# Kernel tuning notes

Measured on AMD Instinct MI355X. Metric: run time of the kernel, lower is better.

## Reference

```python
import jax, jax.numpy as jnp
import numpy as np

B, S, A, H, Z = 256, 512, 64, 1024, 256

def setup_inputs() -> dict:
    key = jax.random.key(0)
    ks = jax.random.split(key, 24)
    w = lambda k, shape: (jax.random.normal(k, shape, jnp.float32) * 0.02)
    inp = {
        "x": jax.random.randint(ks[0], (B, S), 0, A),
        "h0": jax.random.normal(ks[1], (B, H), jnp.float32),            # init_hidden randn
        "eps": jax.random.normal(ks[2], (S + 1, B, Z), jnp.float32),     # reparam noise per step + final
        "phi_x_w": w(ks[3], (H, A)),  "phi_x_b": jnp.zeros((H,), jnp.float32),
        "enc_w1": w(ks[4], (H, 2 * H)), "enc_b1": jnp.zeros((H,), jnp.float32),
        "enc_w2": w(ks[5], (Z, H)),     "enc_b2": jnp.zeros((Z,), jnp.float32),
        "pri_w1": w(ks[6], (H, H)),     "pri_b1": jnp.zeros((H,), jnp.float32),
        "pri_w2": w(ks[7], (Z, H)),     "pri_b2": jnp.zeros((Z,), jnp.float32),
        "phi_z_w": w(ks[8], (H, Z)),    "phi_z_b": jnp.zeros((H,), jnp.float32),
        "dec_w": w(ks[9], (H, 2 * H)),  "dec_b": jnp.zeros((H,), jnp.float32),
        "act_w": w(ks[10], (A, H)),     "act_b": jnp.zeros((A,), jnp.float32),
        "gru_wih": w(ks[11], (3 * H, 2 * H)), "gru_whh": w(ks[12], (3 * H, H)),
        "gru_bih": jnp.zeros((3 * H,), jnp.float32), "gru_bhh": jnp.zeros((3 * H,), jnp.float32),
    }
    return inp

def reference(x, h0, eps, phi_x_w, phi_x_b, enc_w1, enc_b1, enc_w2, enc_b2,
              pri_w1, pri_b1, pri_w2, pri_b2, phi_z_w, phi_z_b, dec_w, dec_b,
              act_w, act_b, gru_wih, gru_whh, gru_bih, gru_bhh):
    relu, sp = jax.nn.relu, jax.nn.softplus

    def gru_cell(xin, h):  # PyTorch GRU gate math
        gi = xin @ gru_wih.T + gru_bih
        gh = h @ gru_whh.T + gru_bhh
        ir, iz, inn = jnp.split(gi, 3, axis=-1)
        hr, hz, hn = jnp.split(gh, 3, axis=-1)
        r = jax.nn.sigmoid(ir + hr)
        zg = jax.nn.sigmoid(iz + hz)
        n = jnp.tanh(inn + r * hn)
        return (1.0 - zg) * n + zg * h

    def prior(h):
        p = relu(h @ pri_w1.T + pri_b1) @ pri_w2.T + pri_b2
        return p, sp(p)

    x_oh = jax.nn.one_hot(x, A, dtype=jnp.float32).transpose(1, 0, 2)  # [S,B,A]

    def step(carry, inp):
        h, kld = carry
        x_t, eps_t = inp
        px = relu(x_t @ phi_x_w.T + phi_x_b)                            # [B,H]
        enc = relu(jnp.concatenate([px, h], -1) @ enc_w1.T + enc_b1) @ enc_w2.T + enc_b2
        enc_std = sp(enc)
        pri_m, pri_std = prior(h)
        kld_el = (2 * jnp.log(pri_std) - 2 * jnp.log(enc_std)
                  + (enc_std ** 2 + (enc - pri_m) ** 2) / pri_std ** 2 - 1.0)
        kld = kld + 0.5 * jnp.sum(kld_el)
        z_t = eps_t * enc_std + enc                                     # reparam sample
        pz = relu(z_t @ phi_z_w.T + phi_z_b)
        h_new = gru_cell(jnp.concatenate([px, pz], -1), h)
        return (h_new, kld), None

    (h, kld), _ = jax.lax.scan(step, (h0, jnp.float32(0.0)), (x_oh, eps[:S]))

    pri_m, pri_std = prior(h)
    z_t = eps[S] * pri_std + pri_m
    pz = relu(z_t @ phi_z_w.T + phi_z_b)
    dec = relu(jnp.concatenate([pz, h], -1) @ dec_w.T + dec_b)
    pred_act = dec @ act_w.T + act_b
    return pred_act, kld
```

## Files before the change

kernel.cpp:

```cpp
#include <hip/hip_runtime.h>


typedef float f32x4 __attribute__((ext_vector_type(4)));
typedef __bf16 bf16x8 __attribute__((ext_vector_type(8)));

#define BB 256
#define SS 512
#define HH 1024
#define ZZ 256
#define AA 64
#define NWG 256

__device__ __forceinline__ float softplus_(float x) {
    return (x > 15.f) ? x : log1pf(expf(x));
}
__device__ __forceinline__ float sigmoid_(float x) {
    return 1.f / (1.f + expf(-x));
}

__device__ __forceinline__ void gbar(unsigned* bar, unsigned p, int wg) {
    __syncthreads();
    if (threadIdx.x == 0) {
        unsigned s = p & 7u;
        unsigned exp = (p >> 3) + 1u;
        unsigned* leaf = bar + (s * 8 + (wg >> 5)) * 16;
        unsigned* root = bar + (64 + s) * 16;
        unsigned* flag = bar + (72 + s) * 16;
        unsigned old = __hip_atomic_fetch_add(leaf, 1u, __ATOMIC_ACQ_REL, __HIP_MEMORY_SCOPE_AGENT);
        if (old == 32u * exp - 1u) {
            unsigned old2 = __hip_atomic_fetch_add(root, 1u, __ATOMIC_ACQ_REL, __HIP_MEMORY_SCOPE_AGENT);
            if (old2 == 8u * exp - 1u) {
                __hip_atomic_store(flag, exp, __ATOMIC_RELEASE, __HIP_MEMORY_SCOPE_AGENT);
            }
        }
        while (__hip_atomic_load(flag, __ATOMIC_ACQUIRE, __HIP_MEMORY_SCOPE_AGENT) < exp) {
            __builtin_amdgcn_s_sleep(2);
        }
    }
    __syncthreads();
}

__device__ __forceinline__ void xbar(unsigned* flags, int g, int rank, int ngrp,
                                     unsigned tok) {
    __syncthreads();
    if (threadIdx.x == 0)
        __hip_atomic_store(flags + g * 256 + rank, tok, __ATOMIC_RELAXED,
                           __HIP_MEMORY_SCOPE_AGENT);
    unsigned l = threadIdx.x & 63;
    unsigned* base = flags + g * 256;
    for (;;) {
        bool ok = true;
        for (int i = (int)l; i < ngrp; i += 64)
            ok &= (__hip_atomic_load(base + i, __ATOMIC_RELAXED,
                                     __HIP_MEMORY_SCOPE_AGENT) >= tok);
        if (__all(ok)) break;
        __builtin_amdgcn_s_sleep(2);
    }
    asm volatile("buffer_inv sc0" ::: "memory");
}

template<int MT, int NT>
__device__ __forceinline__ void wgemm(const __bf16* __restrict__ A, int lda, int mstride,
                                      const __bf16* __restrict__ B, int ldb, int nstride,
                                      int K, f32x4 (&acc)[MT][NT]) {
    int lane = threadIdx.x & 63;
    int rr = lane & 15;
    int ko = (lane >> 4) * 8;
    const __bf16* ap = A + rr * lda + ko;
    const __bf16* bp = B + rr * ldb + ko;
    #pragma unroll 2
    for (int k = 0; k < K; k += 32) {
        bf16x8 af[MT], bfr[NT];
        #pragma unroll
        for (int mt = 0; mt < MT; mt++) af[mt] = *(const bf16x8*)(ap + mt * mstride + k);
        #pragma unroll
        for (int nt = 0; nt < NT; nt++) bfr[nt] = *(const bf16x8*)(bp + nt * nstride + k);
        #pragma unroll
        for (int mt = 0; mt < MT; mt++)
            #pragma unroll
            for (int nt = 0; nt < NT; nt++)
                acc[mt][nt] = __builtin_amdgcn_mfma_f32_16x16x32_bf16(af[mt], bfr[nt], acc[mt][nt], 0, 0, 0);
    }
}


__global__ void k_zeroctl(unsigned* bar, unsigned* flags, unsigned* cnt, float* kldacc) {
    for (int i = threadIdx.x; i < 1280; i += 256) bar[i] = 0u;
    for (int i = threadIdx.x; i < 2048; i += 256) flags[i] = 0u;
    if (threadIdx.x < 8) cnt[threadIdx.x] = 0u;
    if (threadIdx.x == 0) *kldacc = 0.f;
}

__global__ void k_pack(const float* __restrict__ src, int src_ld, int col_off,
                       __bf16* __restrict__ dst, int cols, int total) {
    int i = blockIdx.x * 256 + threadIdx.x;
    if (i >= total) return;
    int r = i / cols, c = i - r * cols;
    dst[i] = (__bf16)src[r * src_ld + col_off + c];
}

__global__ void k_copyf(const float* __restrict__ s, float* __restrict__ d, int n) {
    int i = blockIdx.x * 256 + threadIdx.x;
    if (i < n) d[i] = s[i];
}

__global__ void k_px(const float* __restrict__ phi_x_w, const float* __restrict__ phi_x_b,
                     float* __restrict__ px) {
    int i = blockIdx.x * 256 + threadIdx.x;
    int a = i >> 10, hh = i & 1023;
    px[i] = fmaxf(phi_x_w[hh * AA + a] + phi_x_b[hh], 0.f);
}

__global__ __launch_bounds__(256) void k_tables(const float* __restrict__ enc_w1,
                                                const float* __restrict__ wih,
                                                const float* __restrict__ px,
                                                float* __restrict__ encpx,
                                                float* __restrict__ gipx) {
    __shared__ float spx[64][65];
    int tid = threadIdx.x;
    int cg = blockIdx.x * 4 + (tid >> 6);
    int a = tid & 63;
    const float* wrow = (cg < 1024) ? (enc_w1 + cg * 2048) : (wih + (cg - 1024) * 2048);
    float sum = 0.f;
    for (int k0 = 0; k0 < 1024; k0 += 64) {
        __syncthreads();
        for (int e = tid; e < 4096; e += 256)
            spx[e >> 6][e & 63] = px[((e >> 6) << 10) + k0 + (e & 63)];
        __syncthreads();
        #pragma unroll 8
        for (int kk = 0; kk < 64; kk++) sum += wrow[k0 + kk] * spx[a][kk];
    }
    if (cg < 1024) encpx[a * 1024 + cg] = sum;
    else gipx[a * 3072 + (cg - 1024)] = sum;
}


struct PArgs {
    const int* x; const float* eps;
    const __bf16 *WA, *W2, *WPZ, *WIH, *WHH, *WDEC, *WACT;
    const float *encpx, *gipx;
    const float *eb1, *pb1, *eb2, *pb2, *pzb, *decb, *actb, *bih, *bhh;
    float *hf0, *hf1; __bf16 *hb0, *hb1;
    __bf16 *hidcat, *zbuf, *pzbuf, *tailhid, *decbuf;
    float *gh; float *kldacc; unsigned *bar, *flags, *cnt;
    float* out;
};

__global__ __launch_bounds__(256) void k_persist(PArgs a) {
    int wg = blockIdx.x;
    int tid = threadIdx.x;
    int v = tid >> 6;
    int lane = tid & 63;
    int rr = lane & 15;
    int ko = (lane >> 4) * 8;
    int col = lane & 15, rq = (lane >> 4) * 4;
    float kl = 0.f;
    float* hf[2] = {a.hf0, a.hf1};
    __bf16* hb[2] = {a.hb0, a.hb1};

    __shared__ float lds2[4][2][256];
    __shared__ int sh_g, sh_rank, sh_ngrp;
    __shared__ float sh_kl[4];

    if (tid == 0) {
        unsigned xcc = __builtin_amdgcn_s_getreg((31 << 11) | (0 << 6) | 20) & 7u;
        sh_g = (int)xcc;
        sh_rank = (int)atomicAdd(a.cnt + xcc, 1u);
    }
    __syncthreads();
    int g = sh_g, rank = sh_rank;
    gbar(a.bar, 0, wg);
    if (tid == 0)
        sh_ngrp = (int)__hip_atomic_load(a.cnt + g, __ATOMIC_RELAXED,
                                         __HIP_MEMORY_SCOPE_AGENT);
    __syncthreads();
    int ngrp = sh_ngrp;
    int base_m = g * 32;

    unsigned tok = 1;

    for (int t = 0; t < SS; t++) {
        int cur = t & 1, nxt = cur ^ 1;

        for (int r = rank; r < 32; r += ngrp) {
            int mt = v >> 1;
            int nt0 = r * 10 + (v & 1) * 5;
            const __bf16* ap = hb[cur] + (size_t)(base_m + mt * 16 + rr) * HH + ko;
            const __bf16* bp[5];
            #pragma unroll
            for (int j = 0; j < 5; j++) {
                int n = (nt0 + j) * 16 + rr;
                bp[j] = ((n < 2048) ? (a.WA + (size_t)n * HH)
                                    : (a.WHH + (size_t)(n - 2048) * HH)) + ko;
            }
            f32x4 acc[5] = {};
            #pragma unroll 2
            for (int k = 0; k < HH; k += 32) {
                bf16x8 af = *(const bf16x8*)(ap + k);
                #pragma unroll
                for (int j = 0; j < 5; j++)
                    acc[j] = __builtin_amdgcn_mfma_f32_16x16x32_bf16(
                        af, *(const bf16x8*)(bp[j] + k), acc[j], 0, 0, 0);
            }
            int xb[4];
            #pragma unroll
            for (int i = 0; i < 4; i++)
                xb[i] = a.x[(base_m + mt * 16 + rq + i) * SS + t];
            #pragma unroll
            for (int j = 0; j < 5; j++) {
                int c0 = (nt0 + j) * 16 + col;
                if (c0 < 1024) {
                    float bias = a.eb1[c0];
                    #pragma unroll
                    for (int i = 0; i < 4; i++) {
                        int m = base_m + mt * 16 + rq + i;
                        float val = acc[j][i] + bias + a.encpx[xb[i] * 1024 + c0];
                        a.hidcat[m * 2048 + c0] = (__bf16)fmaxf(val, 0.f);
                    }
                } else if (c0 < 2048) {
                    float bias = a.pb1[c0 - 1024];
                    #pragma unroll
                    for (int i = 0; i < 4; i++) {
                        int m = base_m + mt * 16 + rq + i;
                        a.hidcat[m * 2048 + c0] = (__bf16)fmaxf(acc[j][i] + bias, 0.f);
                    }
                } else {
                    int gc = c0 - 2048;
                    #pragma unroll
                    for (int i = 0; i < 4; i++) {
                        int m = base_m + mt * 16 + rq + i;
                        a.gh[m * 3072 + gc] = acc[j][i];
                    }
                }
            }
        }
        xbar(a.flags, g, rank, ngrp, tok++);

        for (int r = rank; r < 32; r += ngrp) {
            int mtl = r >> 4, zsl = r & 15;
            const __bf16* ae_p = a.hidcat + (size_t)(base_m + mtl * 16 + rr) * 2048 + v * 256 + ko;
            const __bf16* ap_p = ae_p + 1024;
            const __bf16* be_p = a.W2 + (size_t)(zsl * 16 + rr) * HH + v * 256 + ko;
            const __bf16* bp_p = a.W2 + (size_t)(256 + zsl * 16 + rr) * HH + v * 256 + ko;
            f32x4 ae = {0.f,0.f,0.f,0.f}, av = {0.f,0.f,0.f,0.f};
            #pragma unroll
            for (int k = 0; k < 256; k += 32) {
                ae = __builtin_amdgcn_mfma_f32_16x16x32_bf16(
                    *(const bf16x8*)(ae_p + k), *(const bf16x8*)(be_p + k), ae, 0, 0, 0);
                av = __builtin_amdgcn_mfma_f32_16x16x32_bf16(
                    *(const bf16x8*)(ap_p + k), *(const bf16x8*)(bp_p + k), av, 0, 0, 0);
            }
            #pragma unroll
            for (int i = 0; i < 4; i++) {
                int idx = (rq + i) * 16 + col;
                lds2[v][0][idx] = ae[i];
                lds2[v][1][idx] = av[i];
            }
            __syncthreads();
            {
                float e = lds2[0][0][tid] + lds2[1][0][tid] + lds2[2][0][tid] + lds2[3][0][tid];
                float pv = lds2[0][1][tid] + lds2[1][1][tid] + lds2[2][1][tid] + lds2[3][1][tid];
                int m = base_m + mtl * 16 + (tid >> 4);
                int z = zsl * 16 + (tid & 15);
                float enc = e + a.eb2[z];
                float pri = pv + a.pb2[z];
                float es = softplus_(enc), ps = softplus_(pri);
                float d = enc - pri;
                kl += 2.f * (logf(ps) - logf(es)) + (es * es + d * d) / (ps * ps) - 1.f;
                const float* epst = a.eps + (size_t)t * BB * ZZ;
                a.zbuf[m * ZZ + z] = (__bf16)(epst[m * ZZ + z] * es + enc);
            }
            __syncthreads();
        }
        xbar(a.flags, g, rank, ngrp, tok++);

        for (int r = rank; r < 32; r += ngrp) {
            int mt = v >> 1;
            int nt = r * 2 + (v & 1);
            const __bf16* ap = a.zbuf + (size_t)(base_m + mt * 16 + rr) * ZZ + ko;
            const __bf16* bp = a.WPZ + (size_t)(nt * 16 + rr) * ZZ + ko;
            f32x4 acc = {0.f,0.f,0.f,0.f};
            #pragma unroll
            for (int k = 0; k < ZZ; k += 32)
                acc = __builtin_amdgcn_mfma_f32_16x16x32_bf16(
                    *(const bf16x8*)(ap + k), *(const bf16x8*)(bp + k), acc, 0, 0, 0);
            int n = nt * 16 + col;
            float b = a.pzb[n];
            #pragma unroll
            for (int i = 0; i < 4; i++) {
                int m = base_m + mt * 16 + rq + i;
                a.pzbuf[m * HH + n] = (__bf16)fmaxf(acc[i] + b, 0.f);
            }
        }
        xbar(a.flags, g, rank, ngrp, tok++);

        for (int r = rank; r < 32; r += ngrp) {
            int mt = v >> 1;
            int jt = r * 2 + (v & 1);
            const __bf16* ap = a.pzbuf + (size_t)(base_m + mt * 16 + rr) * HH + ko;
            const __bf16* bp0 = a.WIH + (size_t)(jt * 16 + rr) * HH + ko;
            const __bf16* bp1g = bp0 + (size_t)1024 * HH;
            const __bf16* bp2g = bp0 + (size_t)2048 * HH;
            f32x4 acc[3] = {};
            #pragma unroll 2
            for (int k = 0; k < HH; k += 32) {
                bf16x8 af = *(const bf16x8*)(ap + k);
                acc[0] = __builtin_amdgcn_mfma_f32_16x16x32_bf16(af, *(const bf16x8*)(bp0 + k), acc[0], 0, 0, 0);
                acc[1] = __builtin_amdgcn_mfma_f32_16x16x32_bf16(af, *(const bf16x8*)(bp1g + k), acc[1], 0, 0, 0);
                acc[2] = __builtin_amdgcn_mfma_f32_16x16x32_bf16(af, *(const bf16x8*)(bp2g + k), acc[2], 0, 0, 0);
            }
            int j = jt * 16 + col;
            float br = a.bih[j], bz2 = a.bih[1024 + j], bn = a.bih[2048 + j];
            float cr = a.bhh[j], cz = a.bhh[1024 + j], cn = a.bhh[2048 + j];
            #pragma unroll
            for (int i = 0; i < 4; i++) {
                int m = base_m + mt * 16 + rq + i;
                int xb = a.x[m * SS + t];
                const float* gp = a.gipx + xb * 3072;
                float gir = acc[0][i] + gp[j] + br;
                float giz = acc[1][i] + gp[1024 + j] + bz2;
                float gin = acc[2][i] + gp[2048 + j] + bn;
                float ghr = a.gh[m * 3072 + j] + cr;
                float ghz = a.gh[m * 3072 + 1024 + j] + cz;
                float ghn = a.gh[m * 3072 + 2048 + j] + cn;
                float rg = sigmoid_(gir + ghr);
                float zg = sigmoid_(giz + ghz);
                float nn = tanhf(gin + rg * ghn);
                float hv = (1.f - zg) * nn + zg * hf[cur][m * HH + j];
                hf[nxt][m * HH + j] = hv;
                hb[nxt][m * HH + j] = (__bf16)hv;
            }
        }
        xbar(a.flags, g, rank, ngrp, tok++);
    }

    for (int r = rank; r < 32; r += ngrp) {
        int mt = v >> 1, nt = r * 2 + (v & 1);
        f32x4 acc[1][1] = {};
        wgemm<1, 1>(hb[0] + (size_t)(base_m + mt * 16) * HH, HH, 0,
                    a.WA + (size_t)(1024 + nt * 16) * HH, HH, 0, HH, acc);
        int n = nt * 16 + col;
        float b = a.pb1[n];
        #pragma unroll
        for (int i = 0; i < 4; i++) {
            int m = base_m + mt * 16 + rq + i;
            a.tailhid[m * HH + n] = (__bf16)fmaxf(acc[0][0][i] + b, 0.f);
        }
    }
    xbar(a.flags, g, rank, ngrp, tok++);
    if (v == 0) {
        for (int r = rank; r < 32; r += ngrp) {
            int mtl = r >> 4, zt = r & 15;
            f32x4 apv[1][1] = {};
            wgemm<1, 1>(a.tailhid + (size_t)(base_m + mtl * 16) * HH, HH, 0,
                        a.W2 + (size_t)(256 + zt * 16) * HH, HH, 0, HH, apv);
            int z = zt * 16 + col;
            float bp = a.pb2[z];
            const float* epst = a.eps + (size_t)SS * BB * ZZ;
            #pragma unroll
            for (int i = 0; i < 4; i++) {
                int m = base_m + mtl * 16 + rq + i;
                float pri = apv[0][0][i] + bp;
                float ps = softplus_(pri);
                a.zbuf[m * ZZ + z] = (__bf16)(epst[m * ZZ + z] * ps + pri);
            }
        }
    }
    xbar(a.flags, g, rank, ngrp, tok++);
    for (int r = rank; r < 32; r += ngrp) {
        int mt = v >> 1, nt = r * 2 + (v & 1);
        f32x4 acc[1][1] = {};
        wgemm<1, 1>(a.zbuf + (size_t)(base_m + mt * 16) * ZZ, ZZ, 0,
                    a.WPZ + (size_t)(nt * 16) * ZZ, ZZ, 0, ZZ, acc);
        int n = nt * 16 + col;
        float b = a.pzb[n];
        #pragma unroll
        for (int i = 0; i < 4; i++) {
            int m = base_m + mt * 16 + rq + i;
            a.pzbuf[m * HH + n] = (__bf16)fmaxf(acc[0][0][i] + b, 0.f);
        }
    }
    xbar(a.flags, g, rank, ngrp, tok++);
    for (int r = rank; r < 32; r += ngrp) {
        int mt = v >> 1, nt = r * 2 + (v & 1);
        f32x4 acc[1][1] = {};
        wgemm<1, 1>(a.pzbuf + (size_t)(base_m + mt * 16) * HH, HH, 0,
                    a.WDEC + (size_t)(nt * 16) * 2048, 2048, 0, HH, acc);
        wgemm<1, 1>(hb[0] + (size_t)(base_m + mt * 16) * HH, HH, 0,
                    a.WDEC + (size_t)(nt * 16) * 2048 + 1024, 2048, 0, HH, acc);
        int n = nt * 16 + col;
        float b = a.decb[n];
        #pragma unroll
        for (int i = 0; i < 4; i++) {
            int m = base_m + mt * 16 + rq + i;
            a.decbuf[m * HH + n] = (__bf16)fmaxf(acc[0][0][i] + b, 0.f);
        }
    }
    xbar(a.flags, g, rank, ngrp, tok++);
    if (v == 0) {
        for (int r = rank; r < 32; r += ngrp) {
            if (r >= 8) continue;
            int mt = r >> 2, nt = r & 3;
            f32x4 acc[1][1] = {};
            wgemm<1, 1>(a.decbuf + (size_t)(base_m + mt * 16) * HH, HH, 0,
                        a.WACT + (size_t)(nt * 16) * HH, HH, 0, HH, acc);
            int n = nt * 16 + col;
            float b = a.actb[n];
            #pragma unroll
            for (int i = 0; i < 4; i++) {
                int m = base_m + mt * 16 + rq + i;
                a.out[m * AA + n] = acc[0][0][i] + b;
            }
        }
    }

    {
        float s = kl;
        #pragma unroll
        for (int off = 1; off < 64; off <<= 1) s += __shfl_xor(s, off);
        if (lane == 0) sh_kl[v] = s;
        __syncthreads();
        if (tid == 0) {
            float ws = sh_kl[0] + sh_kl[1] + sh_kl[2] + sh_kl[3];
            atomicAdd(a.kldacc, ws);
        }
    }
    gbar(a.bar, 1, wg);
    if (wg == 0 && tid == 0) {
        float s = __hip_atomic_load(a.kldacc, __ATOMIC_ACQUIRE, __HIP_MEMORY_SCOPE_AGENT);
        a.out[BB * AA] = 0.5f * s;
    }
}

extern "C" void kernel_launch(void* const* d_in, const int* in_sizes, int n_in,
                              void* d_out, int out_size, void* d_ws, size_t ws_size,
                              hipStream_t stream) {
    const int*   x       = (const int*)d_in[0];
    const float* h0      = (const float*)d_in[1];
    const float* eps     = (const float*)d_in[2];
    const float* phi_x_w = (const float*)d_in[3];
    const float* phi_x_b = (const float*)d_in[4];
    const float* enc_w1  = (const float*)d_in[5];
    const float* enc_b1  = (const float*)d_in[6];
    const float* enc_w2  = (const float*)d_in[7];
    const float* enc_b2  = (const float*)d_in[8];
    const float* pri_w1  = (const float*)d_in[9];
    const float* pri_b1  = (const float*)d_in[10];
    const float* pri_w2  = (const float*)d_in[11];
    const float* pri_b2  = (const float*)d_in[12];
    const float* phi_z_w = (const float*)d_in[13];
    const float* phi_z_b = (const float*)d_in[14];
    const float* dec_w   = (const float*)d_in[15];
    const float* dec_b   = (const float*)d_in[16];
    const float* act_w   = (const float*)d_in[17];
    const float* act_b   = (const float*)d_in[18];
    const float* gru_wih = (const float*)d_in[19];
    const float* gru_whh = (const float*)d_in[20];
    const float* gru_bih = (const float*)d_in[21];
    const float* gru_bhh = (const float*)d_in[22];

    char* p = (char*)d_ws;
    auto alloc = [&](size_t bytes) { char* r = p; p += (bytes + 255) & ~(size_t)255; return r; };

    __bf16* WA    = (__bf16*)alloc(2048 * 1024 * 2);
    __bf16* W2    = (__bf16*)alloc(512 * 1024 * 2);
    __bf16* WPZ   = (__bf16*)alloc(1024 * 256 * 2);
    __bf16* WIH   = (__bf16*)alloc(3072 * 1024 * 2);
    __bf16* WHH   = (__bf16*)alloc(3072 * 1024 * 2);
    __bf16* WDEC  = (__bf16*)alloc(1024 * 2048 * 2);
    __bf16* WACT  = (__bf16*)alloc(64 * 1024 * 2);
    float*  px    = (float*)alloc(64 * 1024 * 4);
    float*  encpx = (float*)alloc(64 * 1024 * 4);
    float*  gipx  = (float*)alloc(64 * 3072 * 4);
    float*  hf0   = (float*)alloc(BB * HH * 4);
    float*  hf1   = (float*)alloc(BB * HH * 4);
    __bf16* hb0   = (__bf16*)alloc(BB * HH * 2);
    __bf16* hb1   = (__bf16*)alloc(BB * HH * 2);
    __bf16* hidcat = (__bf16*)alloc(BB * 2048 * 2);
    __bf16* zbuf   = (__bf16*)alloc(BB * ZZ * 2);
    __bf16* pzbuf  = (__bf16*)alloc(BB * HH * 2);
    __bf16* tailhid = (__bf16*)alloc(BB * HH * 2);
    __bf16* decbuf  = (__bf16*)alloc(BB * HH * 2);
    float*  gh     = (float*)alloc(BB * 3072 * 4);
    unsigned* bar  = (unsigned*)alloc(1280 * 4);
    unsigned* flags = (unsigned*)alloc(2048 * 4);
    unsigned* cnt  = (unsigned*)alloc(64 * 4);
    float*  kldacc = (float*)alloc(256);

    auto pack = [&](const float* src, int src_ld, int off, __bf16* dst, int rows, int cols) {
        int total = rows * cols;
        k_pack<<<(total + 255) / 256, 256, 0, stream>>>(src, src_ld, off, dst, cols, total);
    };

    k_zeroctl<<<1, 256, 0, stream>>>(bar, flags, cnt, kldacc);
    pack(enc_w1, 2048, 1024, WA, 1024, 1024);
    pack(pri_w1, 1024, 0, WA + 1024 * 1024, 1024, 1024);
    pack(enc_w2, 1024, 0, W2, 256, 1024);
    pack(pri_w2, 1024, 0, W2 + 256 * 1024, 256, 1024);
    pack(phi_z_w, 256, 0, WPZ, 1024, 256);
    pack(gru_wih, 2048, 1024, WIH, 3072, 1024);
    pack(gru_whh, 1024, 0, WHH, 3072, 1024);
    pack(dec_w, 2048, 0, WDEC, 1024, 2048);
    pack(act_w, 1024, 0, WACT, 64, 1024);
    pack(h0, 1024, 0, hb0, 256, 1024);
    k_copyf<<<(BB * HH + 255) / 256, 256, 0, stream>>>(h0, hf0, BB * HH);
    k_px<<<(64 * 1024) / 256, 256, 0, stream>>>(phi_x_w, phi_x_b, px);
    k_tables<<<1024, 256, 0, stream>>>(enc_w1, gru_wih, px, encpx, gipx);

    PArgs pa;
    pa.x = x; pa.eps = eps;
// ... 16 lines not shown
```

Baseline: 29.21 ms.

## Double persistent workgroups and split recurrent GEMM tiles across more blocks

Raises the persistent grid from 256 to 512 workgroups with two blocks per CU, and rescales the tree barrier's leaf fan-in to match. The first per-step GEMM is repartitioned into 64 tiles of 5 column blocks, with waves alternating between 3 and 2 tiles. The GRU input GEMM splits K across wave pairs and reduces the halves through shared memory. The goal is more parallelism and latency hiding in each serial step, at the cost of more barrier participants, extra syncthreads, and register pressure from the 2-block launch bound.

After: 48.47 ms. 1.66x slower.

```diff
diff --git a/kernel.cpp b/kernel.cpp
--- a/kernel.cpp
+++ b/kernel.cpp
@@ -9,7 +9,7 @@
 #define HH 1024
 #define ZZ 256
 #define AA 64
-#define NWG 256
+#define NWG 512
 
 __device__ __forceinline__ float softplus_(float x) {
     return (x > 15.f) ? x : log1pf(expf(x));
@@ -23,11 +23,11 @@
     if (threadIdx.x == 0) {
         unsigned s = p & 7u;
         unsigned exp = (p >> 3) + 1u;
-        unsigned* leaf = bar + (s * 8 + (wg >> 5)) * 16;
+        unsigned* leaf = bar + (s * 8 + (wg >> 6)) * 16;
         unsigned* root = bar + (64 + s) * 16;
         unsigned* flag = bar + (72 + s) * 16;
         unsigned old = __hip_atomic_fetch_add(leaf, 1u, __ATOMIC_ACQ_REL, __HIP_MEMORY_SCOPE_AGENT);
-        if (old == 32u * exp - 1u) {
+        if (old == 64u * exp - 1u) {
             unsigned old2 = __hip_atomic_fetch_add(root, 1u, __ATOMIC_ACQ_REL, __HIP_MEMORY_SCOPE_AGENT);
             if (old2 == 8u * exp - 1u) {
                 __hip_atomic_store(flag, exp, __ATOMIC_RELEASE, __HIP_MEMORY_SCOPE_AGENT);
@@ -146,7 +146,7 @@
     float* out;
 };
 
-__global__ __launch_bounds__(256) void k_persist(PArgs a) {
+__global__ __launch_bounds__(256, 2) void k_persist(PArgs a) {
     int wg = blockIdx.x;
     int tid = threadIdx.x;
     int v = tid >> 6;
@@ -159,6 +159,7 @@
     __bf16* hb[2] = {a.hb0, a.hb1};
 
     __shared__ float lds2[4][2][256];
+    __shared__ float ldsP4[2][3][256];
     __shared__ int sh_g, sh_rank, sh_ngrp;
     __shared__ float sh_kl[4];
 
@@ -182,32 +183,46 @@
     for (int t = 0; t < SS; t++) {
         int cur = t & 1, nxt = cur ^ 1;
 
-        for (int r = rank; r < 32; r += ngrp) {
+        for (int r = rank; r < 64; r += ngrp) {
             int mt = v >> 1;
-            int nt0 = r * 10 + (v & 1) * 5;
+            int hv = (v ^ r) & 1;
+            int NT = hv ? 2 : 3;
+            int nt0 = r * 5 + (hv ? 3 : 0);
             const __bf16* ap = hb[cur] + (size_t)(base_m + mt * 16 + rr) * HH + ko;
-            const __bf16* bp[5];
-            #pragma unroll
-            for (int j = 0; j < 5; j++) {
-                int n = (nt0 + j) * 16 + rr;
-                bp[j] = ((n < 2048) ? (a.WA + (size_t)n * HH)
-                                    : (a.WHH + (size_t)(n - 2048) * HH)) + ko;
-            }
-            f32x4 acc[5] = {};
-            #pragma unroll 2
-            for (int k = 0; k < HH; k += 32) {
-                bf16x8 af = *(const bf16x8*)(ap + k);
-                #pragma unroll
-                for (int j = 0; j < 5; j++)
-                    acc[j] = __builtin_amdgcn_mfma_f32_16x16x32_bf16(
-                        af, *(const bf16x8*)(bp[j] + k), acc[j], 0, 0, 0);
+            int n0 = (nt0 + 0) * 16 + rr;
+            int n1 = (nt0 + 1) * 16 + rr;
+            const __bf16* bp0 = ((n0 < 2048) ? (a.WA + (size_t)n0 * HH)
+                                             : (a.WHH + (size_t)(n0 - 2048) * HH)) + ko;
+            const __bf16* bp1 = ((n1 < 2048) ? (a.WA + (size_t)n1 * HH)
+                                             : (a.WHH + (size_t)(n1 - 2048) * HH)) + ko;
+            const __bf16* bp2 = bp0;
+            if (NT == 3) {
+                int n2 = (nt0 + 2) * 16 + rr;
+                bp2 = ((n2 < 2048) ? (a.WA + (size_t)n2 * HH)
+                                   : (a.WHH + (size_t)(n2 - 2048) * HH)) + ko;
+            }
+            f32x4 acc[3] = {};
+            if (NT == 3) {
+                #pragma unroll 4
+                for (int k = 0; k < HH; k += 32) {
+                    bf16x8 af = *(const bf16x8*)(ap + k);
+                    acc[0] = __builtin_amdgcn_mfma_f32_16x16x32_bf16(af, *(const bf16x8*)(bp0 + k), acc[0], 0, 0, 0);
+                    acc[1] = __builtin_amdgcn_mfma_f32_16x16x32_bf16(af, *(const bf16x8*)(bp1 + k), acc[1], 0, 0, 0);
+                    acc[2] = __builtin_amdgcn_mfma_f32_16x16x32_bf16(af, *(const bf16x8*)(bp2 + k), acc[2], 0, 0, 0);
+                }
+            } else {
+                #pragma unroll 4
+                for (int k = 0; k < HH; k += 32) {
+                    bf16x8 af = *(const bf16x8*)(ap + k);
+                    acc[0] = __builtin_amdgcn_mfma_f32_16x16x32_bf16(af, *(const bf16x8*)(bp0 + k), acc[0], 0, 0, 0);
+                    acc[1] = __builtin_amdgcn_mfma_f32_16x16x32_bf16(af, *(const bf16x8*)(bp1 + k), acc[1], 0, 0, 0);
+                }
             }
             int xb[4];
             #pragma unroll
             for (int i = 0; i < 4; i++)
                 xb[i] = a.x[(base_m + mt * 16 + rq + i) * SS + t];
-            #pragma unroll
-            for (int j = 0; j < 5; j++) {
+            for (int j = 0; j < NT; j++) {
                 int c0 = (nt0 + j) * 16 + col;
                 if (c0 < 1024) {
                     float bias = a.eb1[c0];
@@ -294,42 +309,59 @@
         }
         xbar(a.flags, g, rank, ngrp, tok++);
 
-        for (int r = rank; r < 32; r += ngrp) {
+        for (int r = rank; r < 64; r += ngrp) {
             int mt = v >> 1;
-            int jt = r * 2 + (v & 1);
-            const __bf16* ap = a.pzbuf + (size_t)(base_m + mt * 16 + rr) * HH + ko;
-            const __bf16* bp0 = a.WIH + (size_t)(jt * 16 + rr) * HH + ko;
+            int kh = v & 1;
+            int jt = r;
+            const __bf16* ap = a.pzbuf + (size_t)(base_m + mt * 16 + rr) * HH + kh * 512 + ko;
+            const __bf16* bp0 = a.WIH + (size_t)(jt * 16 + rr) * HH + kh * 512 + ko;
             const __bf16* bp1g = bp0 + (size_t)1024 * HH;
             const __bf16* bp2g = bp0 + (size_t)2048 * HH;
             f32x4 acc[3] = {};
-            #pragma unroll 2
-            for (int k = 0; k < HH; k += 32) {
+            #pragma unroll 4
+            for (int k = 0; k < 512; k += 32) {
                 bf16x8 af = *(const bf16x8*)(ap + k);
                 acc[0] = __builtin_amdgcn_mfma_f32_16x16x32_bf16(af, *(const bf16x8*)(bp0 + k), acc[0], 0, 0, 0);
                 acc[1] = __builtin_amdgcn_mfma_f32_16x16x32_bf16(af, *(const bf16x8*)(bp1g + k), acc[1], 0, 0, 0);
                 acc[2] = __builtin_amdgcn_mfma_f32_16x16x32_bf16(af, *(const bf16x8*)(bp2g + k), acc[2], 0, 0, 0);
             }
-            int j = jt * 16 + col;
-            float br = a.bih[j], bz2 = a.bih[1024 + j], bn = a.bih[2048 + j];
-            float cr = a.bhh[j], cz = a.bhh[1024 + j], cn = a.bhh[2048 + j];
-            #pragma unroll
-            for (int i = 0; i < 4; i++) {
-                int m = base_m + mt * 16 + rq + i;
-                int xb = a.x[m * SS + t];
-                const float* gp = a.gipx + xb * 3072;
-                float gir = acc[0][i] + gp[j] + br;
-                float giz = acc[1][i] + gp[1024 + j] + bz2;
-                float gin = acc[2][i] + gp[2048 + j] + bn;
-                float ghr = a.gh[m * 3072 + j] + cr;
-                float ghz = a.gh[m * 3072 + 1024 + j] + cz;
-                float ghn = a.gh[m * 3072 + 2048 + j] + cn;
-                float rg = sigmoid_(gir + ghr);
-                float zg = sigmoid_(giz + ghz);
-                float nn = tanhf(gin + rg * ghn);
-                float hv = (1.f - zg) * nn + zg * hf[cur][m * HH + j];
-                hf[nxt][m * HH + j] = hv;
-                hb[nxt][m * HH + j] = (__bf16)hv;
-            }
+            if (kh) {
+                #pragma unroll
+                for (int g3 = 0; g3 < 3; g3++)
+                    #pragma unroll
+                    for (int i = 0; i < 4; i++)
+                        ldsP4[mt][g3][(rq + i) * 16 + col] = acc[g3][i];
+            }
+            __syncthreads();
+            if (!kh) {
+                #pragma unroll
+                for (int g3 = 0; g3 < 3; g3++)
+                    #pragma unroll
+                    for (int i = 0; i < 4; i++)
+                        acc[g3][i] += ldsP4[mt][g3][(rq + i) * 16 + col];
+                int j = jt * 16 + col;
+                float br = a.bih[j], bz2 = a.bih[1024 + j], bn = a.bih[2048 + j];
+                float cr = a.bhh[j], cz = a.bhh[1024 + j], cn = a.bhh[2048 + j];
+                #pragma unroll
+                for (int i = 0; i < 4; i++) {
+                    int m = base_m + mt * 16 + rq + i;
+                    int xb = a.x[m * SS + t];
+                    const float* gp = a.gipx + xb * 3072;
+                    float gir = acc[0][i] + gp[j] + br;
+                    float giz = acc[1][i] + gp[1024 + j] + bz2;
+                    float gin = acc[2][i] + gp[2048 + j] + bn;
+                    float ghr = a.gh[m * 3072 + j] + cr;
+                    float ghz = a.gh[m * 3072 + 1024 + j] + cz;
+                    float ghn = a.gh[m * 3072 + 2048 + j] + cn;
+                    float rg = sigmoid_(gir + ghr);
+                    float zg = sigmoid_(giz + ghz);
+                    float nn = tanhf(gin + rg * ghn);
+                    float hv2 = (1.f - zg) * nn + zg * hf[cur][m * HH + j];
+                    hf[nxt][m * HH + j] = hv2;
+                    hb[nxt][m * HH + j] = (__bf16)hv2;
+                }
+            }
+            __syncthreads();
         }
         xbar(a.flags, g, rank, ngrp, tok++);
     }
```

## Split K across waves with LDS reduction to reuse B fragments over two M tiles

Applied to the files above, without the earlier changes.

In the two big per-step GEMM phases (hidden projection and GRU input gates), each wave now covers both 16-row M tiles and half of K instead of one M tile and the full K. Each B fragment loaded from global memory therefore feeds two MFMAs. Partial sums are exchanged through a new 20KB LDS buffer and the epilogue work is split across the two K halves. This halves weight traffic per MFMA but adds LDS traffic, extra __syncthreads, and more accumulator registers. It also sets launch bounds to one block per CU.

Result: faster. 27.86 ms (-4.6%).

```diff
diff --git a/kernel.cpp b/kernel.cpp
--- a/kernel.cpp
+++ b/kernel.cpp
@@ -146,7 +146,7 @@
     float* out;
 };
 
-__global__ __launch_bounds__(256) void k_persist(PArgs a) {
+__global__ __launch_bounds__(256, 1) void k_persist(PArgs a) {
     int wg = blockIdx.x;
     int tid = threadIdx.x;
     int v = tid >> 6;
@@ -158,6 +158,7 @@
     float* hf[2] = {a.hf0, a.hf1};
     __bf16* hb[2] = {a.hb0, a.hb1};
 
+    __shared__ float ldsC[5120];
     __shared__ float lds2[4][2][256];
     __shared__ int sh_g, sh_rank, sh_ngrp;
     __shared__ float sh_kl[4];
@@ -183,56 +184,84 @@
         int cur = t & 1, nxt = cur ^ 1;
 
         for (int r = rank; r < 32; r += ngrp) {
-            int mt = v >> 1;
-            int nt0 = r * 10 + (v & 1) * 5;
-            const __bf16* ap = hb[cur] + (size_t)(base_m + mt * 16 + rr) * HH + ko;
+            int nh = v & 1, kh = v >> 1;
+            int nt0 = r * 10 + nh * 5;
+            const __bf16* ap0 = hb[cur] + (size_t)(base_m + rr) * HH + kh * 512 + ko;
+            const __bf16* ap1 = ap0 + (size_t)16 * HH;
             const __bf16* bp[5];
             #pragma unroll
             for (int j = 0; j < 5; j++) {
                 int n = (nt0 + j) * 16 + rr;
                 bp[j] = ((n < 2048) ? (a.WA + (size_t)n * HH)
-                                    : (a.WHH + (size_t)(n - 2048) * HH)) + ko;
-            }
-            f32x4 acc[5] = {};
-            #pragma unroll 2
-            for (int k = 0; k < HH; k += 32) {
-                bf16x8 af = *(const bf16x8*)(ap + k);
+                                    : (a.WHH + (size_t)(n - 2048) * HH)) + kh * 512 + ko;
+            }
+            f32x4 acc[2][5] = {};
+            #pragma unroll 4
+            for (int k = 0; k < 512; k += 32) {
+                bf16x8 a0 = *(const bf16x8*)(ap0 + k);
+                bf16x8 a1 = *(const bf16x8*)(ap1 + k);
                 #pragma unroll
-                for (int j = 0; j < 5; j++)
-                    acc[j] = __builtin_amdgcn_mfma_f32_16x16x32_bf16(
-                        af, *(const bf16x8*)(bp[j] + k), acc[j], 0, 0, 0);
-            }
-            int xb[4];
-            #pragma unroll
-            for (int i = 0; i < 4; i++)
-                xb[i] = a.x[(base_m + mt * 16 + rq + i) * SS + t];
-            #pragma unroll
-            for (int j = 0; j < 5; j++) {
+                for (int j = 0; j < 5; j++) {
+                    bf16x8 bb = *(const bf16x8*)(bp[j] + k);
+                    acc[0][j] = __builtin_amdgcn_mfma_f32_16x16x32_bf16(a0, bb, acc[0][j], 0, 0, 0);
+                    acc[1][j] = __builtin_amdgcn_mfma_f32_16x16x32_bf16(a1, bb, acc[1][j], 0, 0, 0);
+                }
+            }
+            {
+                int wlo = kh ? 0 : 3, whi = kh ? 3 : 5;
+                for (int j = wlo; j < whi; j++)
+                    #pragma unroll
+                    for (int mt = 0; mt < 2; mt++)
+                        #pragma unroll
+                        for (int i = 0; i < 4; i++)
+                            ldsC[((nh * 5 + j) * 2 + mt) * 256 + (rq + i) * 16 + col] = acc[mt][j][i];
+            }
+            int xbv[2][4];
+            #pragma unroll
+            for (int mt = 0; mt < 2; mt++)
+                #pragma unroll
+                for (int i = 0; i < 4; i++)
+                    xbv[mt][i] = a.x[(base_m + mt * 16 + rq + i) * SS + t];
+            __syncthreads();
+            int jlo = kh ? 3 : 0, jhi = kh ? 5 : 3;
+            for (int j = jlo; j < jhi; j++) {
+                #pragma unroll
+                for (int mt = 0; mt < 2; mt++)
+                    #pragma unroll
+                    for (int i = 0; i < 4; i++)
+                        acc[mt][j][i] += ldsC[((nh * 5 + j) * 2 + mt) * 256 + (rq + i) * 16 + col];
                 int c0 = (nt0 + j) * 16 + col;
                 if (c0 < 1024) {
                     float bias = a.eb1[c0];
                     #pragma unroll
-                    for (int i = 0; i < 4; i++) {
-                        int m = base_m + mt * 16 + rq + i;
-                        float val = acc[j][i] + bias + a.encpx[xb[i] * 1024 + c0];
-                        a.hidcat[m * 2048 + c0] = (__bf16)fmaxf(val, 0.f);
-                    }
+                    for (int mt = 0; mt < 2; mt++)
+                        #pragma unroll
+                        for (int i = 0; i < 4; i++) {
+                            int m = base_m + mt * 16 + rq + i;
+                            float val = acc[mt][j][i] + bias + a.encpx[xbv[mt][i] * 1024 + c0];
+                            a.hidcat[m * 2048 + c0] = (__bf16)fmaxf(val, 0.f);
+                        }
                 } else if (c0 < 2048) {
                     float bias = a.pb1[c0 - 1024];
                     #pragma unroll
-                    for (int i = 0; i < 4; i++) {
-                        int m = base_m + mt * 16 + rq + i;
-                        a.hidcat[m * 2048 + c0] = (__bf16)fmaxf(acc[j][i] + bias, 0.f);
-                    }
+                    for (int mt = 0; mt < 2; mt++)
+                        #pragma unroll
+                        for (int i = 0; i < 4; i++) {
+                            int m = base_m + mt * 16 + rq + i;
+                            a.hidcat[m * 2048 + c0] = (__bf16)fmaxf(acc[mt][j][i] + bias, 0.f);
+                        }
                 } else {
                     int gc = c0 - 2048;
                     #pragma unroll
-                    for (int i = 0; i < 4; i++) {
-                        int m = base_m + mt * 16 + rq + i;
-                        a.gh[m * 3072 + gc] = acc[j][i];
-                    }
+                    for (int mt = 0; mt < 2; mt++)
+                        #pragma unroll
+                        for (int i = 0; i < 4; i++) {
+                            int m = base_m + mt * 16 + rq + i;
+                            a.gh[m * 3072 + gc] = acc[mt][j][i];
+                        }
                 }
             }
+            __syncthreads();
         }
         xbar(a.flags, g, rank, ngrp, tok++);
 
@@ -295,41 +324,67 @@
         xbar(a.flags, g, rank, ngrp, tok++);
 
         for (int r = rank; r < 32; r += ngrp) {
-            int mt = v >> 1;
-            int jt = r * 2 + (v & 1);
-            const __bf16* ap = a.pzbuf + (size_t)(base_m + mt * 16 + rr) * HH + ko;
-            const __bf16* bp0 = a.WIH + (size_t)(jt * 16 + rr) * HH + ko;
+            int jh = v & 1, kh = v >> 1;
+            int jt = r * 2 + jh;
+            const __bf16* ap0 = a.pzbuf + (size_t)(base_m + rr) * HH + kh * 512 + ko;
+            const __bf16* ap1 = ap0 + (size_t)16 * HH;
+            const __bf16* bp0 = a.WIH + (size_t)(jt * 16 + rr) * HH + kh * 512 + ko;
             const __bf16* bp1g = bp0 + (size_t)1024 * HH;
             const __bf16* bp2g = bp0 + (size_t)2048 * HH;
-            f32x4 acc[3] = {};
-            #pragma unroll 2
-            for (int k = 0; k < HH; k += 32) {
-                bf16x8 af = *(const bf16x8*)(ap + k);
-                acc[0] = __builtin_amdgcn_mfma_f32_16x16x32_bf16(af, *(const bf16x8*)(bp0 + k), acc[0], 0, 0, 0);
-                acc[1] = __builtin_amdgcn_mfma_f32_16x16x32_bf16(af, *(const bf16x8*)(bp1g + k), acc[1], 0, 0, 0);
-                acc[2] = __builtin_amdgcn_mfma_f32_16x16x32_bf16(af, *(const bf16x8*)(bp2g + k), acc[2], 0, 0, 0);
-            }
-            int j = jt * 16 + col;
-            float br = a.bih[j], bz2 = a.bih[1024 + j], bn = a.bih[2048 + j];
-            float cr = a.bhh[j], cz = a.bhh[1024 + j], cn = a.bhh[2048 + j];
-            #pragma unroll
-            for (int i = 0; i < 4; i++) {
-                int m = base_m + mt * 16 + rq + i;
-                int xb = a.x[m * SS + t];
-                const float* gp = a.gipx + xb * 3072;
-                float gir = acc[0][i] + gp[j] + br;
-                float giz = acc[1][i] + gp[1024 + j] + bz2;
-                float gin = acc[2][i] + gp[2048 + j] + bn;
-                float ghr = a.gh[m * 3072 + j] + cr;
-                float ghz = a.gh[m * 3072 + 1024 + j] + cz;
-                float ghn = a.gh[m * 3072 + 2048 + j] + cn;
-                float rg = sigmoid_(gir + ghr);
-                float zg = sigmoid_(giz + ghz);
-                float nn = tanhf(gin + rg * ghn);
-                float hv = (1.f - zg) * nn + zg * hf[cur][m * HH + j];
-                hf[nxt][m * HH + j] = hv;
-                hb[nxt][m * HH + j] = (__bf16)hv;
-            }
+            f32x4 acc[2][3] = {};
+            #pragma unroll 4
+            for (int k = 0; k < 512; k += 32) {
+                bf16x8 a0 = *(const bf16x8*)(ap0 + k);
+                bf16x8 a1 = *(const bf16x8*)(ap1 + k);
+                bf16x8 b0 = *(const bf16x8*)(bp0 + k);
+                bf16x8 b1 = *(const bf16x8*)(bp1g + k);
+                bf16x8 b2 = *(const bf16x8*)(bp2g + k);
+                acc[0][0] = __builtin_amdgcn_mfma_f32_16x16x32_bf16(a0, b0, acc[0][0], 0, 0, 0);
+                acc[0][1] = __builtin_amdgcn_mfma_f32_16x16x32_bf16(a0, b1, acc[0][1], 0, 0, 0);
+                acc[0][2] = __builtin_amdgcn_mfma_f32_16x16x32_bf16(a0, b2, acc[0][2], 0, 0, 0);
+                acc[1][0] = __builtin_amdgcn_mfma_f32_16x16x32_bf16(a1, b0, acc[1][0], 0, 0, 0);
+                acc[1][1] = __builtin_amdgcn_mfma_f32_16x16x32_bf16(a1, b1, acc[1][1], 0, 0, 0);
+                acc[1][2] = __builtin_amdgcn_mfma_f32_16x16x32_bf16(a1, b2, acc[1][2], 0, 0, 0);
+            }
+            {
+                int mtW = kh ^ 1;
+                #pragma unroll
+                for (int g3 = 0; g3 < 3; g3++)
+                    #pragma unroll
+                    for (int i = 0; i < 4; i++)
+                        ldsC[((jh * 2 + mtW) * 3 + g3) * 256 + (rq + i) * 16 + col] = acc[mtW][g3][i];
+            }
+            __syncthreads();
+            {
+                int mt = kh;
+                #pragma unroll
+                for (int g3 = 0; g3 < 3; g3++)
+                    #pragma unroll
+                    for (int i = 0; i < 4; i++)
+                        acc[mt][g3][i] += ldsC[((jh * 2 + mt) * 3 + g3) * 256 + (rq + i) * 16 + col];
+                int j = jt * 16 + col;
+                float br = a.bih[j], bz2 = a.bih[1024 + j], bn = a.bih[2048 + j];
+                float cr = a.bhh[j], cz = a.bhh[1024 + j], cn = a.bhh[2048 + j];
+                #pragma unroll
+                for (int i = 0; i < 4; i++) {
+                    int m = base_m + mt * 16 + rq + i;
+                    int xb = a.x[m * SS + t];
+                    const float* gp = a.gipx + xb * 3072;
+                    float gir = acc[mt][0][i] + gp[j] + br;
+                    float giz = acc[mt][1][i] + gp[1024 + j] + bz2;
+                    float gin = acc[mt][2][i] + gp[2048 + j] + bn;
+                    float ghr = a.gh[m * 3072 + j] + cr;
+                    float ghz = a.gh[m * 3072 + 1024 + j] + cz;
+                    float ghn = a.gh[m * 3072 + 2048 + j] + cn;
+                    float rg = sigmoid_(gir + ghr);
+                    float zg = sigmoid_(giz + ghz);
+                    float nn = tanhf(gin + rg * ghn);
+                    float hv = (1.f - zg) * nn + zg * hf[cur][m * HH + j];
+                    hf[nxt][m * HH + j] = hv;
+                    hb[nxt][m * HH + j] = (__bf16)hv;
+                }
+            }
+            __syncthreads();
         }
         xbar(a.flags, g, rank, ngrp, tok++);
     }
```

## Repartition GEMMs by output columns per XCC with grid barriers and LDS A-tiles

Applied to the files above, without the earlier changes.

Changes the work split so each XCC group owns a slice of output columns (weights) for all 256 batch rows instead of a slice of batch rows for all columns. Per-group flag barriers become a global tree barrier with relaxed atomics plus a cache invalidate. Shared activations are now written with cache-bypassing stores and read with atomic loads. The A tile is staged into LDS. The aim is to keep each XCC's weight slice resident in its own L2 and cut redundant weight traffic. The cost is a grid-wide barrier every phase and cross-XCC activation exchange.

After: 32.39 ms. 10.9% more time.

```diff
diff --git a/kernel.cpp b/kernel.cpp
--- a/kernel.cpp
+++ b/kernel.cpp
@@ -3,6 +3,8 @@
 
 typedef float f32x4 __attribute__((ext_vector_type(4)));
 typedef __bf16 bf16x8 __attribute__((ext_vector_type(8)));
+typedef unsigned long long u64;
+typedef u64 u64x2 __attribute__((ext_vector_type(2)));
 
 #define BB 256
 #define SS 512
@@ -18,7 +20,19 @@
     return 1.f / (1.f + expf(-x));
 }
 
-__device__ __forceinline__ void gbar(unsigned* bar, unsigned p, int wg) {
+__device__ __forceinline__ u64 ld8a(const __bf16* p) {
+    return __hip_atomic_load((const u64*)p, __ATOMIC_RELAXED, __HIP_MEMORY_SCOPE_AGENT);
+}
+__device__ __forceinline__ bf16x8 ld16a(const __bf16* p) {
+    u64x2 t; t.x = ld8a(p); t.y = ld8a(p + 4);
+    return __builtin_bit_cast(bf16x8, t);
+}
+__device__ __forceinline__ void st2a(__bf16* p, float v) {
+    unsigned w = __builtin_bit_cast(unsigned short, (__bf16)v);
+    asm volatile("global_store_short %0, %1, off sc0 sc1" :: "v"(p), "v"(w) : "memory");
+}
+
+__device__ __forceinline__ void gbarR(unsigned* bar, unsigned p, int wg) {
     __syncthreads();
     if (threadIdx.x == 0) {
         unsigned s = p & 7u;
@@ -26,17 +40,16 @@
         unsigned* leaf = bar + (s * 8 + (wg >> 5)) * 16;
         unsigned* root = bar + (64 + s) * 16;
         unsigned* flag = bar + (72 + s) * 16;
-        unsigned old = __hip_atomic_fetch_add(leaf, 1u, __ATOMIC_ACQ_REL, __HIP_MEMORY_SCOPE_AGENT);
+        unsigned old = __hip_atomic_fetch_add(leaf, 1u, __ATOMIC_RELAXED, __HIP_MEMORY_SCOPE_AGENT);
         if (old == 32u * exp - 1u) {
-            unsigned old2 = __hip_atomic_fetch_add(root, 1u, __ATOMIC_ACQ_REL, __HIP_MEMORY_SCOPE_AGENT);
-            if (old2 == 8u * exp - 1u) {
-                __hip_atomic_store(flag, exp, __ATOMIC_RELEASE, __HIP_MEMORY_SCOPE_AGENT);
-            }
-        }
-        while (__hip_atomic_load(flag, __ATOMIC_ACQUIRE, __HIP_MEMORY_SCOPE_AGENT) < exp) {
+            unsigned old2 = __hip_atomic_fetch_add(root, 1u, __ATOMIC_RELAXED, __HIP_MEMORY_SCOPE_AGENT);
+            if (old2 == 8u * exp - 1u)
+                __hip_atomic_store(flag, exp, __ATOMIC_RELAXED, __HIP_MEMORY_SCOPE_AGENT);
+        }
+        while (__hip_atomic_load(flag, __ATOMIC_RELAXED, __HIP_MEMORY_SCOPE_AGENT) < exp)
             __builtin_amdgcn_s_sleep(2);
-        }
-    }
+    }
+    asm volatile("buffer_inv sc0" ::: "memory");
     __syncthreads();
 }
 
@@ -57,6 +70,7 @@
         __builtin_amdgcn_s_sleep(2);
     }
     asm volatile("buffer_inv sc0" ::: "memory");
+    __syncthreads();
 }
 
 template<int MT, int NT>
@@ -146,7 +160,7 @@
     float* out;
 };
 
-__global__ __launch_bounds__(256) void k_persist(PArgs a) {
+__global__ __launch_bounds__(256, 1) void k_persist(PArgs a) {
     int wg = blockIdx.x;
     int tid = threadIdx.x;
     int v = tid >> 6;
@@ -158,6 +172,7 @@
     float* hf[2] = {a.hf0, a.hf1};
     __bf16* hb[2] = {a.hb0, a.hb1};
 
+    __shared__ __align__(16) __bf16 Alds[16][1032];
     __shared__ float lds2[4][2][256];
     __shared__ int sh_g, sh_rank, sh_ngrp;
     __shared__ float sh_kl[4];
@@ -169,7 +184,7 @@
     }
     __syncthreads();
     int g = sh_g, rank = sh_rank;
-    gbar(a.bar, 0, wg);
+    gbarR(a.bar, 0, wg);
     if (tid == 0)
         sh_ngrp = (int)__hip_atomic_load(a.cnt + g, __ATOMIC_RELAXED,
                                          __HIP_MEMORY_SCOPE_AGENT);
@@ -177,26 +192,42 @@
     int ngrp = sh_ngrp;
     int base_m = g * 32;
 
-    unsigned tok = 1;
+    unsigned gp = 1;
 
     for (int t = 0; t < SS; t++) {
         int cur = t & 1, nxt = cur ^ 1;
 
-        for (int r = rank; r < 32; r += ngrp) {
-            int mt = v >> 1;
-            int nt0 = r * 10 + (v & 1) * 5;
-            const __bf16* ap = hb[cur] + (size_t)(base_m + mt * 16 + rr) * HH + ko;
-            const __bf16* bp[5];
+        for (int r0 = rank; r0 < 32; r0 += ngrp) {
+            int mt = r0 & 15;
+            __syncthreads();
+            {
+                const __bf16* src = hb[cur] + (size_t)(mt * 16) * HH + tid * 4;
+                u64 tmp[16];
+                #pragma unroll
+                for (int e2 = 0; e2 < 16; e2++) tmp[e2] = ld8a(src + (size_t)e2 * HH);
+                #pragma unroll
+                for (int e2 = 0; e2 < 16; e2++)
+                    *(u64*)((char*)(&Alds[e2][0]) + tid * 8) = tmp[e2];
+            }
+            __syncthreads();
+            int ntg = (r0 >> 4) + 2 * v;
+            const __bf16* bp[5]; int qv[5];
             #pragma unroll
             for (int j = 0; j < 5; j++) {
-                int n = (nt0 + j) * 16 + rr;
-                bp[j] = ((n < 2048) ? (a.WA + (size_t)n * HH)
-                                    : (a.WHH + (size_t)(n - 2048) * HH)) + ko;
+                int q = ntg * 5 + j; qv[j] = q;
+                const __bf16* b;
+                if (q < 16) b = a.WA + (size_t)(g * 256 + q * 16 + rr) * HH;
+                else {
+                    int qq = q - 16;
+                    b = a.WHH + (size_t)((qq >> 3) * 1024 + g * 128 + (qq & 7) * 16 + rr) * HH;
+                }
+                bp[j] = b + ko;
             }
             f32x4 acc[5] = {};
-            #pragma unroll 2
+            const __bf16* arow = &Alds[rr][ko];
+            #pragma unroll 4
             for (int k = 0; k < HH; k += 32) {
-                bf16x8 af = *(const bf16x8*)(ap + k);
+                bf16x8 af = *(const bf16x8*)(arow + k);
                 #pragma unroll
                 for (int j = 0; j < 5; j++)
                     acc[j] = __builtin_amdgcn_mfma_f32_16x16x32_bf16(
@@ -204,51 +235,59 @@
             }
             int xb[4];
             #pragma unroll
-            for (int i = 0; i < 4; i++)
-                xb[i] = a.x[(base_m + mt * 16 + rq + i) * SS + t];
+            for (int i = 0; i < 4; i++) xb[i] = a.x[(mt * 16 + rq + i) * SS + t];
             #pragma unroll
             for (int j = 0; j < 5; j++) {
-                int c0 = (nt0 + j) * 16 + col;
-                if (c0 < 1024) {
-                    float bias = a.eb1[c0];
-                    #pragma unroll
-                    for (int i = 0; i < 4; i++) {
-                        int m = base_m + mt * 16 + rq + i;
-                        float val = acc[j][i] + bias + a.encpx[xb[i] * 1024 + c0];
-                        a.hidcat[m * 2048 + c0] = (__bf16)fmaxf(val, 0.f);
-                    }
-                } else if (c0 < 2048) {
-                    float bias = a.pb1[c0 - 1024];
-                    #pragma unroll
-                    for (int i = 0; i < 4; i++) {
-                        int m = base_m + mt * 16 + rq + i;
-                        a.hidcat[m * 2048 + c0] = (__bf16)fmaxf(acc[j][i] + bias, 0.f);
+                int q = qv[j];
+                if (q < 16) {
+                    int c = g * 256 + q * 16 + col;
+                    if (c < 1024) {
+                        float bias = a.eb1[c];
+                        #pragma unroll
+                        for (int i = 0; i < 4; i++) {
+                            int m = mt * 16 + rq + i;
+                            float val = acc[j][i] + bias + a.encpx[xb[i] * 1024 + c];
+                            st2a(&a.hidcat[(size_t)m * 2048 + c], fmaxf(val, 0.f));
+                        }
+                    } else {
+                        float bias = a.pb1[c - 1024];
+                        #pragma unroll
+                        for (int i = 0; i < 4; i++) {
+                            int m = mt * 16 + rq + i;
+                            st2a(&a.hidcat[(size_t)m * 2048 + c], fmaxf(acc[j][i] + bias, 0.f));
+                        }
                     }
                 } else {
-                    int gc = c0 - 2048;
+                    int qq = q - 16;
+                    int gc = (qq >> 3) * 1024 + g * 128 + (qq & 7) * 16 + col;
                     #pragma unroll
-                    for (int i = 0; i < 4; i++) {
-                        int m = base_m + mt * 16 + rq + i;
-                        a.gh[m * 3072 + gc] = acc[j][i];
-                    }
+                    for (int i = 0; i < 4; i++)
+                        a.gh[(size_t)(mt * 16 + rq + i) * 3072 + gc] = acc[j][i];
                 }
             }
         }
-        xbar(a.flags, g, rank, ngrp, tok++);
+        gbarR(a.bar, gp++, wg);
 
         for (int r = rank; r < 32; r += ngrp) {
-            int mtl = r >> 4, zsl = r & 15;
-            const __bf16* ae_p = a.hidcat + (size_t)(base_m + mtl * 16 + rr) * 2048 + v * 256 + ko;
+            int mtl = r >> 1;
+            int zsl = g * 2 + (r & 1);
+            const __bf16* ae_p = a.hidcat + (size_t)(mtl * 16 + rr) * 2048 + v * 256 + ko;
             const __bf16* ap_p = ae_p + 1024;
             const __bf16* be_p = a.W2 + (size_t)(zsl * 16 + rr) * HH + v * 256 + ko;
             const __bf16* bp_p = a.W2 + (size_t)(256 + zsl * 16 + rr) * HH + v * 256 + ko;
+            bf16x8 aef[8], apf[8];
+            #pragma unroll
+            for (int k8 = 0; k8 < 8; k8++) {
+                aef[k8] = ld16a(ae_p + k8 * 32);
+                apf[k8] = ld16a(ap_p + k8 * 32);
+            }
             f32x4 ae = {0.f,0.f,0.f,0.f}, av = {0.f,0.f,0.f,0.f};
             #pragma unroll
-            for (int k = 0; k < 256; k += 32) {
+            for (int k8 = 0; k8 < 8; k8++) {
                 ae = __builtin_amdgcn_mfma_f32_16x16x32_bf16(
-                    *(const bf16x8*)(ae_p + k), *(const bf16x8*)(be_p + k), ae, 0, 0, 0);
+                    aef[k8], *(const bf16x8*)(be_p + k8 * 32), ae, 0, 0, 0);
                 av = __builtin_amdgcn_mfma_f32_16x16x32_bf16(
-                    *(const bf16x8*)(ap_p + k), *(const bf16x8*)(bp_p + k), av, 0, 0, 0);
+                    apf[k8], *(const bf16x8*)(bp_p + k8 * 32), av, 0, 0, 0);
             }
             #pragma unroll
             for (int i = 0; i < 4; i++) {
@@ -260,7 +299,7 @@
             {
                 float e = lds2[0][0][tid] + lds2[1][0][tid] + lds2[2][0][tid] + lds2[3][0][tid];
                 float pv = lds2[0][1][tid] + lds2[1][1][tid] + lds2[2][1][tid] + lds2[3][1][tid];
-                int m = base_m + mtl * 16 + (tid >> 4);
+                int m = mtl * 16 + (tid >> 4);
                 int z = zsl * 16 + (tid & 15);
                 float enc = e + a.eb2[z];
                 float pri = pv + a.pb2[z];
@@ -268,72 +307,87 @@
                 float d = enc - pri;
                 kl += 2.f * (logf(ps) - logf(es)) + (es * es + d * d) / (ps * ps) - 1.f;
                 const float* epst = a.eps + (size_t)t * BB * ZZ;
-                a.zbuf[m * ZZ + z] = (__bf16)(epst[m * ZZ + z] * es + enc);
+                st2a(&a.zbuf[(size_t)m * ZZ + z], epst[m * ZZ + z] * es + enc);
             }
             __syncthreads();
         }
-        xbar(a.flags, g, rank, ngrp, tok++);
-
-        for (int r = rank; r < 32; r += ngrp) {
-            int mt = v >> 1;
-            int nt = r * 2 + (v & 1);
-            const __bf16* ap = a.zbuf + (size_t)(base_m + mt * 16 + rr) * ZZ + ko;
-            const __bf16* bp = a.WPZ + (size_t)(nt * 16 + rr) * ZZ + ko;
+        gbarR(a.bar, gp++, wg);
+
+        for (int r0 = rank; r0 < 32; r0 += ngrp) {
+            int mt = r0 & 15;
+            int nt = (r0 >> 4) + 2 * v;
+            const __bf16* apz = a.zbuf + (size_t)(mt * 16 + rr) * ZZ + ko;
+            const __bf16* bpz = a.WPZ + (size_t)((g * 8 + nt) * 16 + rr) * ZZ + ko;
+            bf16x8 azf[8];
+            #pragma unroll
+            for (int k8 = 0; k8 < 8; k8++) azf[k8] = ld16a(apz + k8 * 32);
             f32x4 acc = {0.f,0.f,0.f,0.f};
             #pragma unroll
-            for (int k = 0; k < ZZ; k += 32)
+            for (int k8 = 0; k8 < 8; k8++)
                 acc = __builtin_amdgcn_mfma_f32_16x16x32_bf16(
-                    *(const bf16x8*)(ap + k), *(const bf16x8*)(bp + k), acc, 0, 0, 0);
-            int n = nt * 16 + col;
+                    azf[k8], *(const bf16x8*)(bpz + k8 * 32), acc, 0, 0, 0);
+            int n = (g * 8 + nt) * 16 + col;
             float b = a.pzb[n];
             #pragma unroll
-            for (int i = 0; i < 4; i++) {
-                int m = base_m + mt * 16 + rq + i;
-                a.pzbuf[m * HH + n] = (__bf16)fmaxf(acc[i] + b, 0.f);
-            }
-        }
-        xbar(a.flags, g, rank, ngrp, tok++);
-
-        for (int r = rank; r < 32; r += ngrp) {
-            int mt = v >> 1;
-            int jt = r * 2 + (v & 1);
-            const __bf16* ap = a.pzbuf + (size_t)(base_m + mt * 16 + rr) * HH + ko;
-            const __bf16* bp0 = a.WIH + (size_t)(jt * 16 + rr) * HH + ko;
+            for (int i = 0; i < 4; i++)
+                st2a(&a.pzbuf[(size_t)(mt * 16 + rq + i) * HH + n], fmaxf(acc[i] + b, 0.f));
+        }
+        gbarR(a.bar, gp++, wg);
+
+        for (int r0 = rank; r0 < 32; r0 += ngrp) {
+            int mt = r0 & 15;
+            __syncthreads();
+            {
+                const __bf16* src = a.pzbuf + (size_t)(mt * 16) * HH + tid * 4;
+                u64 tmp[16];
+                #pragma unroll
+                for (int e2 = 0; e2 < 16; e2++) tmp[e2] = ld8a(src + (size_t)e2 * HH);
+                #pragma unroll
+                for (int e2 = 0; e2 < 16; e2++)
+                    *(u64*)((char*)(&Alds[e2][0]) + tid * 8) = tmp[e2];
+            }
+            __syncthreads();
+            int jt = (r0 >> 4) + 2 * v;
+            int jtg = g * 8 + jt;
+            const __bf16* bp0 = a.WIH + (size_t)(jtg * 16 + rr) * HH + ko;
             const __bf16* bp1g = bp0 + (size_t)1024 * HH;
             const __bf16* bp2g = bp0 + (size_t)2048 * HH;
             f32x4 acc[3] = {};
-            #pragma unroll 2
+            const __bf16* arow = &Alds[rr][ko];
+            #pragma unroll 4
             for (int k = 0; k < HH; k += 32) {
-                bf16x8 af = *(const bf16x8*)(ap + k);
+                bf16x8 af = *(const bf16x8*)(arow + k);
                 acc[0] = __builtin_amdgcn_mfma_f32_16x16x32_bf16(af, *(const bf16x8*)(bp0 + k), acc[0], 0, 0, 0);
                 acc[1] = __builtin_amdgcn_mfma_f32_16x16x32_bf16(af, *(const bf16x8*)(bp1g + k), acc[1], 0, 0, 0);
                 acc[2] = __builtin_amdgcn_mfma_f32_16x16x32_bf16(af, *(const bf16x8*)(bp2g + k), acc[2], 0, 0, 0);
             }
-            int j = jt * 16 + col;
+            int j = jtg * 16 + col;
             float br = a.bih[j], bz2 = a.bih[1024 + j], bn = a.bih[2048 + j];
             float cr = a.bhh[j], cz = a.bhh[1024 + j], cn = a.bhh[2048 + j];
             #pragma unroll
             for (int i = 0; i < 4; i++) {
-                int m = base_m + mt * 16 + rq + i;
+                int m = mt * 16 + rq + i;
                 int xb = a.x[m * SS + t];
-                const float* gp = a.gipx + xb * 3072;
-                float gir = acc[0][i] + gp[j] + br;
-                float giz = acc[1][i] + gp[1024 + j] + bz2;
-                float gin = acc[2][i] + gp[2048 + j] + bn;
-                float ghr = a.gh[m * 3072 + j] + cr;
-                float ghz = a.gh[m * 3072 + 1024 + j] + cz;
-                float ghn = a.gh[m * 3072 + 2048 + j] + cn;
+                const float* gpp = a.gipx + (size_t)xb * 3072;
+                const float* ghrow = a.gh + (size_t)m * 3072;
+                float gir = acc[0][i] + gpp[j] + br;
+                float giz = acc[1][i] + gpp[1024 + j] + bz2;
+                float gin = acc[2][i] + gpp[2048 + j] + bn;
+                float ghr = ghrow[j] + cr;
+                float ghz = ghrow[1024 + j] + cz;
+                float ghn = ghrow[2048 + j] + cn;
                 float rg = sigmoid_(gir + ghr);
                 float zg = sigmoid_(giz + ghz);
                 float nn = tanhf(gin + rg * ghn);
-                float hv = (1.f - zg) * nn + zg * hf[cur][m * HH + j];
-                hf[nxt][m * HH + j] = hv;
-                hb[nxt][m * HH + j] = (__bf16)hv;
-            }
-        }
-        xbar(a.flags, g, rank, ngrp, tok++);
-    }
-
+                float hv2 = (1.f - zg) * nn + zg * hf[cur][(size_t)m * HH + j];
+                hf[nxt][(size_t)m * HH + j] = hv2;
+                st2a(&hb[nxt][(size_t)m * HH + j], hv2);
+            }
+        }
+        gbarR(a.bar, gp++, wg);
+    }
+
+    unsigned tok = 1;
     for (int r = rank; r < 32; r += ngrp) {
         int mt = v >> 1, nt = r * 2 + (v & 1);
         f32x4 acc[1][1] = {};
@@ -425,7 +479,7 @@
             atomicAdd(a.kldacc, ws);
         }
     }
-    gbar(a.bar, 1, wg);
+    gbarR(a.bar, gp++, wg);
     if (wg == 0 && tid == 0) {
         float s = __hip_atomic_load(a.kldacc, __ATOMIC_ACQUIRE, __HIP_MEMORY_SCOPE_AGENT);
         a.out[BB * AA] = 0.5f * s;
```
